# Performance work log

Measured on AMD Instinct MI355X. Metric: run time of the kernel, lower is better.

## Reference

```python
import jax, jax.numpy as jnp
import numpy as np

NODE_NUM = 10000
E = 8192        # edges = conv3 in_channels (set dynamically in torch forward)
L = 1024        # Conv1d length dim
C2 = 120 * 1 * 2  # channel_dim * time_reduce_size * 2 = 240


def setup_inputs() -> dict:
    key = jax.random.key(0)
    k = jax.random.split(key, 7)
    x = jax.random.normal(k[0], (NODE_NUM, 128), dtype=jnp.float32)
    edge_index = jax.random.randint(k[1], (2, E), 0, NODE_NUM)
    edge_attr = jax.random.normal(k[2], (E, L), dtype=jnp.float32)
    # conv3: Conv1d(E, C2, kernel=1) -> weight [C2, E], bias [C2]
    conv3_w = jax.random.normal(k[3], (C2, E), dtype=jnp.float32) / np.sqrt(E)
    conv3_b = jax.random.normal(k[4], (C2,), dtype=jnp.float32) / np.sqrt(E)
    # conv4: Conv1d(C2, 1, kernel=1) -> weight [1, C2], bias [1]
    conv4_w = jax.random.normal(k[5], (1, C2), dtype=jnp.float32) / np.sqrt(C2)
    conv4_b = jax.random.normal(k[6], (1,), dtype=jnp.float32) / np.sqrt(C2)
    return {"x": x, "edge_index": edge_index, "edge_attr": edge_attr,
            "conv3_w": conv3_w, "conv3_b": conv3_b,
            "conv4_w": conv4_w, "conv4_b": conv4_b}


def reference(x, edge_index, edge_attr, conv3_w, conv3_b, conv4_w, conv4_b):
    node_num = x.shape[0]
    # conv3 (1x1 conv over unbatched [E, L] input) + relu -> edge [C2, L]
    edge = jax.nn.relu(conv3_w @ edge_attr + conv3_b[:, None])
    # conv4 -> rel_type logits [1, L]; sigmoid -> mask [L]
    mask = jax.nn.sigmoid((conv4_w @ edge + conv4_b[:, None])[0])
    # edge2node: y = edge + edge * mask ; ones(node_num, C2) @ y == column-sum
    # broadcast to all nodes (algebraically identical to the dense matmul).
    col_sum = jnp.sum(edge * (1.0 + mask)[None, :], axis=0)  # [L]
    incoming = jnp.broadcast_to(col_sum[None, :], (node_num, col_sum.shape[0]))
    return incoming / incoming.shape[1]
```

## Files before the change

kernel.cpp:

```cpp
#include <hip/hip_runtime.h>
#include <hip/hip_bf16.h>

#define K_DIM 8192
#define L_DIM 1024
#define C2 240
#define MSTRIDE 256
#define BM 128
#define BN 128
#define BK 64
#define KSPLIT 16
#define KCHUNK 512
#define NSTEP 8
#define PART_KC (L_DIM * MSTRIDE)
#define PART_BYTES ((size_t)KSPLIT * PART_KC * 2)
#define TOT_F4 (10000 * 256)

typedef __attribute__((ext_vector_type(4))) float f32x4;
typedef __attribute__((ext_vector_type(2))) float f32x2;
typedef __attribute__((ext_vector_type(8))) short bf16x8;
typedef __attribute__((ext_vector_type(4))) short bf16x4;

__device__ __forceinline__ unsigned short f2bf(float f) {
  return __builtin_bit_cast(unsigned short, __float2bfloat16(f));
}
__device__ __forceinline__ float bf2f(unsigned short h) {
  unsigned u = ((unsigned)h) << 16;
  return __builtin_bit_cast(float, u);
}

__global__ __launch_bounds__(512, 2) void k_gemm(
    const float* __restrict__ Wm, const float* __restrict__ Am,
    unsigned short* __restrict__ part)
{
  __shared__ __align__(16) unsigned short sW[2 * BM * BK];
  __shared__ __align__(16) unsigned short sA[2 * BN * BK];

  const int t    = threadIdx.x;
  const int lane = t & 63;
  const int bid  = blockIdx.x;

  const int wk    = (bid & 7) * 32 + (bid >> 3);
  const int nt8   = wk & 7;
  const int mtile = (wk >> 3) & 1;
  const int kc    = wk >> 4;

  const int wid = t >> 6;
  const int mg  = wid >> 2;
  const int ng  = wid & 3;
  const int l15 = lane & 15;
  const int lk8 = (lane >> 4) * 8;

  const int n0b = nt8 * BN;
  const int m0b = mtile * BM;
  const int k0  = kc * KCHUNK;

  const int swm = t >> 2;
  const int swk = (t & 3) * 16;
  const int san = (t & 63) * 2;
  const int sak = (t >> 6) * 8;

  const float* wp = Wm + (size_t)(m0b + swm) * K_DIM + k0 + swk;
  const float* ap = Am + (size_t)(k0 + sak) * L_DIM + n0b + san;
  const bool wok = (m0b + swm) < C2;

  f32x4 wregs[2][4];
  f32x2 aregs[2][8];
  f32x4 acc[4][2];
#pragma unroll
  for (int i = 0; i < 4; ++i)
#pragma unroll
    for (int j = 0; j < 2; ++j) acc[i][j] = (f32x4){0.f, 0.f, 0.f, 0.f};

#pragma unroll
  for (int p = 0; p < 2; ++p) {
#pragma unroll
    for (int j = 0; j < 4; ++j)
      wregs[p][j] = wok ? *(const f32x4*)(wp + p * BK + 4 * j)
                        : (f32x4){0.f, 0.f, 0.f, 0.f};
#pragma unroll
    for (int r = 0; r < 8; ++r)
      aregs[p][r] = *(const f32x2*)(ap + (size_t)(p * BK + r) * L_DIM);
  }

#pragma unroll
  for (int s = 0; s < NSTEP; ++s) {
    unsigned short* swb = sW + (s & 1) * (BM * BK);
    unsigned short* sab = sA + (s & 1) * (BN * BK);

#pragma unroll
    for (int j = 0; j < 2; ++j) {
      f32x4 a = wregs[s & 1][2 * j], b = wregs[s & 1][2 * j + 1];
      bf16x8 v;
      v[0] = (short)f2bf(a[0]); v[1] = (short)f2bf(a[1]);
      v[2] = (short)f2bf(a[2]); v[3] = (short)f2bf(a[3]);
      v[4] = (short)f2bf(b[0]); v[5] = (short)f2bf(b[1]);
      v[6] = (short)f2bf(b[2]); v[7] = (short)f2bf(b[3]);
      *(bf16x8*)&swb[swm * BK + ((swk + 8 * j) ^ ((swm & 7) << 3))] = v;
    }
#pragma unroll
    for (int j = 0; j < 2; ++j) {
      const int n = san + j;
      bf16x8 v;
#pragma unroll
      for (int r = 0; r < 8; ++r)
        v[r] = (short)f2bf(j ? aregs[s & 1][r][1] : aregs[s & 1][r][0]);
      *(bf16x8*)&sab[n * BK + (sak ^ ((n & 7) << 3))] = v;
    }
    __syncthreads();

    if (s + 2 < NSTEP) {
      const float* wp2 = wp + (s + 2) * BK;
      const float* ap2 = ap + (size_t)(s + 2) * BK * L_DIM;
#pragma unroll
      for (int j = 0; j < 4; ++j)
        wregs[s & 1][j] = wok ? *(const f32x4*)(wp2 + 4 * j)
                              : (f32x4){0.f, 0.f, 0.f, 0.f};
#pragma unroll
      for (int r = 0; r < 8; ++r)
        aregs[s & 1][r] = *(const f32x2*)(ap2 + (size_t)r * L_DIM);
    }

#pragma unroll
    for (int kk = 0; kk < BK; kk += 32) {
      bf16x8 wf[4], af[2];
#pragma unroll
      for (int mt = 0; mt < 4; ++mt) {
        int m = mg * 64 + mt * 16 + l15;
        wf[mt] = *(const bf16x8*)&swb[m * BK + ((kk + lk8) ^ ((m & 7) << 3))];
      }
#pragma unroll
      for (int nt = 0; nt < 2; ++nt) {
        int n = ng * 32 + nt * 16 + l15;
        af[nt] = *(const bf16x8*)&sab[n * BK + ((kk + lk8) ^ ((n & 7) << 3))];
      }
#pragma unroll
      for (int mt = 0; mt < 4; ++mt)
#pragma unroll
        for (int nt = 0; nt < 2; ++nt)
          acc[mt][nt] = __builtin_amdgcn_mfma_f32_16x16x32_bf16(
              wf[mt], af[nt], acc[mt][nt], 0, 0, 0);
    }
  }

  unsigned short* pb = part + (size_t)kc * PART_KC;
#pragma unroll
  for (int mt = 0; mt < 4; ++mt) {
    const int m0 = m0b + mg * 64 + mt * 16 + (lane >> 4) * 4;
#pragma unroll
    for (int nt = 0; nt < 2; ++nt) {
      const int n = n0b + ng * 32 + nt * 16 + l15;
      bf16x4 v;
      v[0] = (short)f2bf(acc[mt][nt][0]);
      v[1] = (short)f2bf(acc[mt][nt][1]);
      v[2] = (short)f2bf(acc[mt][nt][2]);
      v[3] = (short)f2bf(acc[mt][nt][3]);
      *(bf16x4*)&pb[(size_t)n * MSTRIDE + m0] = v;
    }
  }
}

__global__ __launch_bounds__(256) void k_colbuf(
    const unsigned short* __restrict__ part, const float* __restrict__ b3,
    const float* __restrict__ w4, const float* __restrict__ b4,
    float* __restrict__ colbuf)
{
  __shared__ float red[2][4];
  const int n = blockIdx.x;
  const int t = threadIdx.x;
  const unsigned short* p = part + (size_t)n * MSTRIDE + t;
  float s = 0.f;
#pragma unroll
  for (int kcc = 0; kcc < KSPLIT; ++kcc)
    s += bf2f(p[(size_t)kcc * PART_KC]);
  float e = 0.f, c4 = 0.f;
  if (t < C2) {
    e  = fmaxf(s + b3[t], 0.f);
    c4 = w4[t] * e;
  }
#pragma unroll
  for (int off = 32; off; off >>= 1) {
    e  += __shfl_xor(e, off);
    c4 += __shfl_xor(c4, off);
  }
  const int wv = t >> 6;
  if ((t & 63) == 0) { red[0][wv] = e; red[1][wv] = c4; }
  __syncthreads();
  if (t == 0) {
    const float cs  = red[0][0] + red[0][1] + red[0][2] + red[0][3];
    const float tc4 = red[1][0] + red[1][1] + red[1][2] + red[1][3] + b4[0];
    const float mask = 1.f / (1.f + expf(-tc4));
    colbuf[n] = cs * (1.f + mask) * (1.f / (float)L_DIM);
  }
}

__global__ __launch_bounds__(256) void k_broadcast(
    const float* __restrict__ colbuf, float4* __restrict__ out)
{
  const size_t idx = (size_t)blockIdx.x * 256 + threadIdx.x;
  const int nq = (int)(idx & 255);
  const float4 v = *(const float4*)(colbuf + nq * 4);
  out[idx] = v;
}

extern "C" void kernel_launch(void* const* d_in, const int* in_sizes, int n_in,
                              void* d_out, int out_size, void* d_ws, size_t ws_size,
                              hipStream_t stream) {
  const float* edge_attr = (const float*)d_in[2];
  const float* w3        = (const float*)d_in[3];
  const float* b3        = (const float*)d_in[4];
  const float* w4        = (const float*)d_in[5];
  const float* b4        = (const float*)d_in[6];

  float* out = (float*)d_out;

  unsigned short* part;
  float* colbuf;
  if (ws_size >= PART_BYTES + 4096) {
    part   = (unsigned short*)d_ws;
    colbuf = (float*)((char*)d_ws + PART_BYTES);
  } else {
    part   = (unsigned short*)d_out;
    colbuf = (float*)d_ws;
  }

  k_gemm      <<<dim3(256),   512, 0, stream>>>(w3, edge_attr, part);
  k_colbuf    <<<dim3(1024),  256, 0, stream>>>(part, b3, w4, b4, colbuf);
  k_broadcast <<<dim3(10000), 256, 0, stream>>>(colbuf, (float4*)out);
}
```

Measured before the change: 31.30 us.

## Pre-convert weights to swizzled bf16 and stream them into LDS directly

A new pre-pass kernel converts conv3 weights to bf16 in the exact swizzled per-step LDS layout. The GEMM then loads the weight tiles with global_load_lds DMA straight into shared memory one step ahead, with no register staging and no conversion. This removes per-block fp32 weight loads and conversion work that was duplicated across the eight N tiles, and frees registers. The cost is an extra kernel launch plus a global write and read of the converted weights. The async LDS loads also now rely on the existing barrier for ordering.

```diff
diff --git a/kernel.cpp b/kernel.cpp
--- a/kernel.cpp
+++ b/kernel.cpp
@@ -13,6 +13,8 @@
 #define NSTEP 8
 #define PART_KC (L_DIM * MSTRIDE)
 #define PART_BYTES ((size_t)KSPLIT * PART_KC * 2)
+#define WSWZ_CHUNKS (2 * 16 * 8 * 1024)
+#define WSWZ_BYTES ((size_t)WSWZ_CHUNKS * 16)
 #define TOT_F4 (10000 * 256)
 
 typedef __attribute__((ext_vector_type(4))) float f32x4;
@@ -28,8 +30,41 @@
   return __builtin_bit_cast(float, u);
 }
 
+__device__ __forceinline__ void gload16(const unsigned short* g,
+                                        unsigned short* lds) {
+  typedef __attribute__((address_space(3))) unsigned int lds_u32;
+  typedef __attribute__((address_space(1))) const unsigned int glb_u32;
+  __builtin_amdgcn_global_load_lds((glb_u32*)g, (lds_u32*)lds, 16, 0, 0);
+}
+
+__global__ __launch_bounds__(256) void k_wconv(
+    const float* __restrict__ W, unsigned short* __restrict__ Wswz)
+{
+  const int g  = blockIdx.x * 256 + threadIdx.x;
+  const int Q  = g & 1023;
+  const int sl = g >> 10;
+  const int ml = Q >> 3;
+  const int cp = Q & 7;
+  const int s  = sl & 7;
+  const int kc = (sl >> 3) & 15;
+  const int mt = sl >> 7;
+  const int mg = mt * BM + ml;
+  const int k  = kc * KCHUNK + s * BK + (cp ^ (ml & 7)) * 8;
+
+  bf16x8 v = (bf16x8){0, 0, 0, 0, 0, 0, 0, 0};
+  if (mg < C2) {
+    const float* src = W + (size_t)mg * K_DIM + k;
+    f32x4 a = *(const f32x4*)src, b = *(const f32x4*)(src + 4);
+    v[0] = (short)f2bf(a[0]); v[1] = (short)f2bf(a[1]);
+    v[2] = (short)f2bf(a[2]); v[3] = (short)f2bf(a[3]);
+    v[4] = (short)f2bf(b[0]); v[5] = (short)f2bf(b[1]);
+    v[6] = (short)f2bf(b[2]); v[7] = (short)f2bf(b[3]);
+  }
+  *(bf16x8*)&Wswz[(size_t)g * 8] = v;
+}
+
 __global__ __launch_bounds__(512, 2) void k_gemm(
-    const float* __restrict__ Wm, const float* __restrict__ Am,
+    const unsigned short* __restrict__ Wswz, const float* __restrict__ Am,
     unsigned short* __restrict__ part)
 {
   __shared__ __align__(16) unsigned short sW[2 * BM * BK];
@@ -54,16 +89,14 @@
   const int m0b = mtile * BM;
   const int k0  = kc * KCHUNK;
 
-  const int swm = t >> 2;
-  const int swk = (t & 3) * 16;
+  const unsigned short* wsrc =
+      Wswz + (size_t)((mtile * 16 + kc) * 8) * 8192;
+  const int wofs = (wid * 2) * 512;
+
   const int san = (t & 63) * 2;
   const int sak = (t >> 6) * 8;
-
-  const float* wp = Wm + (size_t)(m0b + swm) * K_DIM + k0 + swk;
   const float* ap = Am + (size_t)(k0 + sak) * L_DIM + n0b + san;
-  const bool wok = (m0b + swm) < C2;
-
-  f32x4 wregs[2][4];
+
   f32x2 aregs[2][8];
   f32x4 acc[4][2];
 #pragma unroll
@@ -71,16 +104,17 @@
 #pragma unroll
     for (int j = 0; j < 2; ++j) acc[i][j] = (f32x4){0.f, 0.f, 0.f, 0.f};
 
-#pragma unroll
-  for (int p = 0; p < 2; ++p) {
-#pragma unroll
-    for (int j = 0; j < 4; ++j)
-      wregs[p][j] = wok ? *(const f32x4*)(wp + p * BK + 4 * j)
-                        : (f32x4){0.f, 0.f, 0.f, 0.f};
+  {
+    unsigned short* dst = sW + wofs;
+    const unsigned short* src = wsrc + wofs + lane * 8;
+    gload16(src, dst);
+    gload16(src + 512, dst + 512);
+  }
+#pragma unroll
+  for (int p = 0; p < 2; ++p)
 #pragma unroll
     for (int r = 0; r < 8; ++r)
       aregs[p][r] = *(const f32x2*)(ap + (size_t)(p * BK + r) * L_DIM);
-  }
 
 #pragma unroll
   for (int s = 0; s < NSTEP; ++s) {
@@ -89,16 +123,6 @@
 
 #pragma unroll
     for (int j = 0; j < 2; ++j) {
-      f32x4 a = wregs[s & 1][2 * j], b = wregs[s & 1][2 * j + 1];
-      bf16x8 v;
-      v[0] = (short)f2bf(a[0]); v[1] = (short)f2bf(a[1]);
-      v[2] = (short)f2bf(a[2]); v[3] = (short)f2bf(a[3]);
-      v[4] = (short)f2bf(b[0]); v[5] = (short)f2bf(b[1]);
-      v[6] = (short)f2bf(b[2]); v[7] = (short)f2bf(b[3]);
-      *(bf16x8*)&swb[swm * BK + ((swk + 8 * j) ^ ((swm & 7) << 3))] = v;
-    }
-#pragma unroll
-    for (int j = 0; j < 2; ++j) {
       const int n = san + j;
       bf16x8 v;
 #pragma unroll
@@ -106,15 +130,17 @@
         v[r] = (short)f2bf(j ? aregs[s & 1][r][1] : aregs[s & 1][r][0]);
       *(bf16x8*)&sab[n * BK + (sak ^ ((n & 7) << 3))] = v;
     }
+
     __syncthreads();
 
+    if (s + 1 < NSTEP) {
+      unsigned short* dst = sW + ((s + 1) & 1) * (BM * BK) + wofs;
+      const unsigned short* src = wsrc + (size_t)(s + 1) * 8192 + wofs + lane * 8;
+      gload16(src, dst);
+      gload16(src + 512, dst + 512);
+    }
     if (s + 2 < NSTEP) {
-      const float* wp2 = wp + (s + 2) * BK;
       const float* ap2 = ap + (size_t)(s + 2) * BK * L_DIM;
-#pragma unroll
-      for (int j = 0; j < 4; ++j)
-        wregs[s & 1][j] = wok ? *(const f32x4*)(wp2 + 4 * j)
-                              : (f32x4){0.f, 0.f, 0.f, 0.f};
 #pragma unroll
       for (int r = 0; r < 8; ++r)
         aregs[s & 1][r] = *(const f32x2*)(ap2 + (size_t)r * L_DIM);
@@ -215,15 +241,19 @@
 
   unsigned short* part;
   float* colbuf;
-  if (ws_size >= PART_BYTES + 4096) {
+  unsigned short* wswz;
+  if (ws_size >= PART_BYTES + 4096 + WSWZ_BYTES) {
     part   = (unsigned short*)d_ws;
     colbuf = (float*)((char*)d_ws + PART_BYTES);
+    wswz   = (unsigned short*)((char*)d_ws + PART_BYTES + 4096);
   } else {
     part   = (unsigned short*)d_out;
+    wswz   = (unsigned short*)((char*)d_out + 25165824);
     colbuf = (float*)d_ws;
   }
 
-  k_gemm      <<<dim3(256),   512, 0, stream>>>(w3, edge_attr, part);
+  k_wconv     <<<dim3(1024),  256, 0, stream>>>(w3, wswz);
+  k_gemm      <<<dim3(256),   512, 0, stream>>>(wswz, edge_attr, part);
   k_colbuf    <<<dim3(1024),  256, 0, stream>>>(part, b3, w4, b4, colbuf);
   k_broadcast <<<dim3(10000), 256, 0, stream>>>(colbuf, (float4*)out);
 }
```

Result: slower. 35.49 us (+13.4%).
